# Performance work log

Measured on AMD Instinct MI355X. Metric: run time of the kernel, lower is better.

The kernel has to match this reference:

```python
import jax, jax.numpy as jnp
import numpy as np

D_MODEL = 1024
N_HEADS = 16
D_HEAD = D_MODEL // N_HEADS


def setup_inputs() -> dict:
    key = jax.random.key(0)
    k1, k2, k3 = jax.random.split(key, 3)
    B, T = 4, 2048
    x = jax.random.normal(k1, (B, T, D_MODEL), dtype=jnp.float32)
    # torch Linear(d, 3d, bias=False): y = x @ W.T ; we store W already transposed -> [d, 3d]
    w_qkv = jax.random.normal(k2, (D_MODEL, 3 * D_MODEL), dtype=jnp.float32) * (D_MODEL ** -0.5)
    w_proj = jax.random.normal(k3, (D_MODEL, D_MODEL), dtype=jnp.float32) * (D_MODEL ** -0.5)
    return {"x": x, "w_qkv": w_qkv, "w_proj": w_proj}


def reference(x, w_qkv, w_proj):
    B, T, C = x.shape
    H, Dh = N_HEADS, D_HEAD
    qkv = (x @ w_qkv).reshape(B, T, 3, H, Dh)
    q = jnp.transpose(qkv[:, :, 0], (0, 2, 1, 3))  # [B,H,T,Dh]
    k = jnp.transpose(qkv[:, :, 1], (0, 2, 1, 3))
    v = jnp.transpose(qkv[:, :, 2], (0, 2, 1, 3))
    scale = 1.0 / jnp.sqrt(jnp.asarray(Dh, dtype=x.dtype))
    att = jnp.einsum('bhqd,bhkd->bhqk', q, k) * scale  # [B,H,T,T]
    causal = jnp.tril(jnp.ones((T, T), dtype=bool))
    att = jnp.where(causal[None, None], att, jnp.asarray(-jnp.inf, dtype=att.dtype))
    att = jax.nn.softmax(att, axis=-1)
    y = jnp.einsum('bhqk,bhkd->bhqd', att, v)          # [B,H,T,Dh]
    y = jnp.transpose(y, (0, 2, 1, 3)).reshape(B, T, C)
    return y @ w_proj
```

## Files before the change

### kernel.cpp

```cpp
#include <hip/hip_runtime.h>
#include <hip/hip_bf16.h>
#include <cmath>

#define T_SEQ 2048
#define NHEADS 16
#define DHEAD 64
#define DMODEL 1024
#define CQKV 3072

typedef __attribute__((ext_vector_type(8))) short short8;
typedef __attribute__((ext_vector_type(8))) __bf16 bf16x8;
typedef __attribute__((ext_vector_type(4))) float floatx4;

#define LDS_CAST(p) ((__attribute__((address_space(3))) void*)(p))
#define GLB_CAST(p) ((const __attribute__((address_space(1))) void*)(p))

static __device__ __forceinline__ floatx4 mfma_bf16(short8 a, short8 b, floatx4 c) {
  return __builtin_amdgcn_mfma_f32_16x16x32_bf16(
      __builtin_bit_cast(bf16x8, a), __builtin_bit_cast(bf16x8, b), c, 0, 0, 0);
}

static __device__ __forceinline__ short f2bf(float f) {
  union { float f; unsigned u; } x; x.f = f;
  unsigned r = x.u + 0x7FFFu + ((x.u >> 16) & 1u);
  return (short)(r >> 16);
}

static __device__ __forceinline__ float bf2f(short s) {
  return __builtin_bit_cast(float, ((unsigned)(unsigned short)s) << 16);
}

static __device__ __forceinline__ float exp2_(float x) {
#if __has_builtin(__builtin_amdgcn_exp2f)
  return __builtin_amdgcn_exp2f(x);
#else
  return exp2f(x);
#endif
}

static __device__ __forceinline__ bool sniff_is_bf16(const unsigned* __restrict__ x) {
  int cnt = 0;
#pragma unroll
  for (int i = 0; i < 32; ++i) {
    unsigned e = (x[i] >> 7) & 0xFFu;
    cnt += (e >= 0x70u && e <= 0x8Fu) ? 1 : 0;
  }
  return cnt >= 16;
}

static __device__ __forceinline__ short8 load8f32(const char* p, size_t idx) {
  const float4* f = (const float4*)(p + idx * 4);
  float4 a = f[0], b = f[1];
  short8 r;
  r[0] = f2bf(a.x); r[1] = f2bf(a.y); r[2] = f2bf(a.z); r[3] = f2bf(a.w);
  r[4] = f2bf(b.x); r[5] = f2bf(b.y); r[6] = f2bf(b.z); r[7] = f2bf(b.w);
  return r;
}

__global__ __launch_bounds__(256) void conv_x(const char* __restrict__ x,
                                              short* __restrict__ o, int n,
                                              const unsigned* __restrict__ xs) {
  const bool isbf = sniff_is_bf16(xs);
  const int i = (blockIdx.x * 256 + threadIdx.x) * 8;
  if (i >= n) return;
  if (isbf) *(short8*)(o + i) = *(const short8*)((const short*)x + i);
  else      *(short8*)(o + i) = load8f32(x, (size_t)i);
}

__global__ __launch_bounds__(256) void tpose(const char* __restrict__ w,
                                             short* __restrict__ wt, int K, int N,
                                             const unsigned* __restrict__ xs) {
  const bool isbf = sniff_is_bf16(xs);
  __shared__ short tile[32][33];
  const int n0 = blockIdx.x * 32, k0 = blockIdx.y * 32;
  const int tx = threadIdx.x & 31, ty = threadIdx.x >> 5;
#pragma unroll
  for (int i = 0; i < 4; ++i) {
    const int r = ty * 4 + i;
    const size_t off = (size_t)(k0 + r) * N + n0 + tx;
    tile[r][tx] = isbf ? ((const short*)w)[off] : f2bf(((const float*)w)[off]);
  }
  __syncthreads();
#pragma unroll
  for (int i = 0; i < 4; ++i) {
    const int r = ty * 4 + i;
    wt[(size_t)(n0 + r) * K + k0 + tx] = tile[tx][r];
  }
}

__global__ __launch_bounds__(512) void gemm256(const short* __restrict__ A,
                                               const short* __restrict__ Bt,
                                               void* __restrict__ C,
                                               short* __restrict__ C2,
                                               int M, int N, int K, int mode,
                                               const unsigned* __restrict__ xs) {
  const bool out_f32 = (mode == 1) ? !sniff_is_bf16(xs) : false;

  __shared__ short as[2][256 * 64];
  __shared__ short bs[2][256 * 64];
  const int tid = threadIdx.x;
  const int wid = tid >> 6, lane = tid & 63;
  const int quad = lane >> 4, l16 = lane & 15;
  const int wm = wid >> 2, wn = wid & 3;

  const int gx = (int)gridDim.x;
  const int nwg = gx * (int)gridDim.y;
  int bid = (int)blockIdx.y * gx + (int)blockIdx.x;
  bid = (bid & 7) * (nwg >> 3) + (bid >> 3);
  const int m0 = (bid / gx) * 256;
  const int n0 = (bid % gx) * 256;

  const int srl = lane >> 3;
  const int sch = ((lane & 7) ^ srl) * 8;
  const int NT = K >> 6;

#define STAGE_A(t, h, b)                                                          \
  do {                                                                            \
    const int kt_ = (t) << 6;                                                     \
    _Pragma("unroll") for (int j_ = 0; j_ < 2; ++j_) {                            \
      const int row_ = (h) * 128 + j_ * 64 + wid * 8;                             \
      const short* g_ = A + (size_t)(m0 + row_ + srl) * K + kt_ + sch;            \
      __builtin_amdgcn_global_load_lds(GLB_CAST(g_), LDS_CAST(&as[(b)][row_ * 64]), 16, 0, 0); \
    }                                                                             \
  } while (0)

#define STAGE_B(t, h, b)                                                          \
  do {                                                                            \
    const int kt_ = (t) << 6;                                                     \
    _Pragma("unroll") for (int j_ = 0; j_ < 2; ++j_) {                            \
      const int row_ = (h) * 128 + j_ * 64 + wid * 8;                             \
      const short* g_ = Bt + (size_t)(n0 + row_ + srl) * K + kt_ + sch;           \
      __builtin_amdgcn_global_load_lds(GLB_CAST(g_), LDS_CAST(&bs[(b)][row_ * 64]), 16, 0, 0); \
    }                                                                             \
  } while (0)

#define SLOT_(kc) ((((kc) * 4 + quad) ^ (l16 & 7)) * 8)

#define LOAD_A(dst, mh, b)                                                        \
  do {                                                                            \
    _Pragma("unroll") for (int mf_ = 0; mf_ < 4; ++mf_)                           \
    _Pragma("unroll") for (int kc_ = 0; kc_ < 2; ++kc_)                           \
      dst[mf_][kc_] = *(const short8*)&as[(b)][(wm * 128 + (mh) * 64 + mf_ * 16 + l16) * 64 + SLOT_(kc_)]; \
  } while (0)

#define LOAD_B(dst, nh, b)                                                        \
  do {                                                                            \
    _Pragma("unroll") for (int nf_ = 0; nf_ < 2; ++nf_)                           \
    _Pragma("unroll") for (int kc_ = 0; kc_ < 2; ++kc_)                           \
      dst[nf_][kc_] = *(const short8*)&bs[(b)][(wn * 64 + (nh) * 32 + nf_ * 16 + l16) * 64 + SLOT_(kc_)]; \
  } while (0)

#define QMFMA(afrag, bfrag, mh, nh)                                               \
  do {                                                                            \
    __builtin_amdgcn_s_setprio(1);                                                \
    _Pragma("unroll") for (int mf_ = 0; mf_ < 4; ++mf_)                           \
    _Pragma("unroll") for (int nf_ = 0; nf_ < 2; ++nf_)                           \
    _Pragma("unroll") for (int kc_ = 0; kc_ < 2; ++kc_)                           \
      acc[(mh) * 4 + mf_][(nh) * 2 + nf_] =                                       \
          mfma_bf16(afrag[mf_][kc_], bfrag[nf_][kc_], acc[(mh) * 4 + mf_][(nh) * 2 + nf_]); \
    __builtin_amdgcn_s_setprio(0);                                                \
  } while (0)

#define BARW_()                                                                   \
  do {                                                                            \
    __builtin_amdgcn_s_barrier();                                                 \
    asm volatile("s_waitcnt lgkmcnt(0)" ::: "memory");                            \
  } while (0)

  const floatx4 zero4 = {0.f, 0.f, 0.f, 0.f};
  floatx4 acc[8][4];
#pragma unroll
  for (int i = 0; i < 8; ++i)
#pragma unroll
    for (int j = 0; j < 4; ++j) acc[i][j] = zero4;

  STAGE_B(0, 0, 0); STAGE_B(0, 1, 0);
  STAGE_A(0, 0, 0); STAGE_A(0, 1, 0);
  STAGE_B(1, 0, 1); STAGE_B(1, 1, 1);
  asm volatile("s_waitcnt vmcnt(4)" ::: "memory");
  __builtin_amdgcn_s_barrier();

  short8 afr[4][2], bf0[2][2], bf1[2][2];

  for (int t = 0; t < NT; ++t) {
    const int cb = t & 1, nb = cb ^ 1;
    const int tA = (t + 1 < NT) ? t + 1 : NT - 1;
    const int tB = (t + 2 < NT) ? t + 2 : NT - 1;

    LOAD_A(afr, 0, cb);
    LOAD_B(bf0, 0, cb);
    STAGE_A(tA, 0, nb);
    BARW_();
    QMFMA(afr, bf0, 0, 0);
    __builtin_amdgcn_s_barrier();

    LOAD_B(bf1, 1, cb);
    STAGE_A(tA, 1, nb);
    BARW_();
    QMFMA(afr, bf1, 0, 1);
    __builtin_amdgcn_s_barrier();

    LOAD_A(afr, 1, cb);
    STAGE_B(tB, 0, cb);
    BARW_();
    QMFMA(afr, bf1, 1, 1);
    __builtin_amdgcn_s_barrier();

    STAGE_B(tB, 1, cb);
    asm volatile("s_waitcnt vmcnt(4)" ::: "memory");
    BARW_();
    QMFMA(afr, bf0, 1, 0);
    __builtin_amdgcn_s_barrier();
  }
  asm volatile("s_waitcnt vmcnt(0)" ::: "memory");

  const int row0 = m0 + wm * 128 + quad * 4;
  const int col0 = n0 + wn * 64 + l16;
  if (mode == 2 && n0 >= 2048) {
#pragma unroll
    for (int mi = 0; mi < 8; ++mi)
#pragma unroll
      for (int ni = 0; ni < 4; ++ni)
#pragma unroll
        for (int r = 0; r < 4; ++r) {
          const int row = row0 + mi * 16 + r;
          const int col = col0 + ni * 16;
          const int d = col & 63, hh = (col >> 6) - 32;
          const int bb = row >> 11, tq = row & 2047;
          C2[((size_t)(bb * 16 + hh) * 64 + d) * T_SEQ + tq] = f2bf(acc[mi][ni][r]);
        }
  } else {
    const int outN = (mode == 2) ? 2048 : N;
#pragma unroll
    for (int mi = 0; mi < 8; ++mi)
#pragma unroll
      for (int ni = 0; ni < 4; ++ni)
#pragma unroll
        for (int r = 0; r < 4; ++r) {
          const size_t off = (size_t)(row0 + mi * 16 + r) * outN + col0 + ni * 16;
          if (out_f32) ((float*)C)[off] = acc[mi][ni][r];
          else         ((short*)C)[off] = f2bf(acc[mi][ni][r]);
        }
  }
#undef STAGE_A
#undef STAGE_B
#undef SLOT_
#undef LOAD_A
#undef LOAD_B
#undef QMFMA
#undef BARW_
}

__global__ __launch_bounds__(256) void attn(const short* __restrict__ qk,
                                            const short* __restrict__ vT,
                                            short* __restrict__ y) {
  __shared__ short ks[64 * 64];
  __shared__ short vs[64 * 64];
  __shared__ short ps[4][16][72];
  const int tid = threadIdx.x;
  const int wid = tid >> 6, lane = tid & 63;
  const int quad = lane >> 4, l16 = lane & 15;
  const int b = blockIdx.x >> 4, h = blockIdx.x & 15;
  const int q0 = ((int)gridDim.y - 1 - (int)blockIdx.y) * 64;
  const int qw0 = q0 + wid * 16;

  const short* qbase = qk + (size_t)b * T_SEQ * 2048 + h * DHEAD;
  const short* kbase = qbase + DMODEL;
  const short* vtb = vT + (size_t)(b * NHEADS + h) * DHEAD * T_SEQ;
  const float SC = 0.18033688011112042f;

  short8 aq[2];
#pragma unroll
  for (int kc = 0; kc < 2; ++kc) {
    short8 raw = *(const short8*)(qbase + (size_t)(qw0 + l16) * 2048 + kc * 32 + quad * 8);
#pragma unroll
    for (int j = 0; j < 8; ++j) aq[kc][j] = f2bf(bf2f(raw[j]) * SC);
  }

  const floatx4 zero4 = {0.f, 0.f, 0.f, 0.f};
  floatx4 o[4], lacc = zero4;
#pragma unroll
  for (int i = 0; i < 4; ++i) o[i] = zero4;
  const short8 ones8 = {0x3F80, 0x3F80, 0x3F80, 0x3F80, 0x3F80, 0x3F80, 0x3F80, 0x3F80};

  const int srl = lane >> 3;
  const int sch = ((lane & 7) ^ srl) * 8;

  const int kend = q0 + 64;
  for (int kt = 0; kt < kend; kt += 64) {
    __syncthreads();
#pragma unroll
    for (int i = 0; i < 2; ++i) {
      const int row = i * 32 + wid * 8 + srl;
      const short* gk = kbase + (size_t)(kt + row) * 2048 + sch;
      const short* gv = vtb + (size_t)row * T_SEQ + kt + sch;
      __builtin_amdgcn_global_load_lds(GLB_CAST(gk), LDS_CAST(ks + (i * 32 + wid * 8) * 64), 16, 0, 0);
      __builtin_amdgcn_global_load_lds(GLB_CAST(gv), LDS_CAST(vs + (i * 32 + wid * 8) * 64), 16, 0, 0);
    }
    __syncthreads();

    floatx4 s[4];
#pragma unroll
    for (int nt = 0; nt < 4; ++nt) {
      s[nt] = zero4;
#pragma unroll
      for (int kc = 0; kc < 2; ++kc) {
        const int slot = ((kc * 4 + quad) ^ (l16 & 7)) * 8;
        const short8 bk = *(const short8*)&ks[(nt * 16 + l16) * 64 + slot];
        s[nt] = mfma_bf16(aq[kc], bk, s[nt]);
      }
    }

    const bool full = (kt + 63 <= qw0);
#pragma unroll
    for (int nt = 0; nt < 4; ++nt)
#pragma unroll
      for (int r = 0; r < 4; ++r) {
        float p = exp2_(s[nt][r]);
        if (!full) {
          const int key = kt + nt * 16 + l16;
          const int q = qw0 + quad * 4 + r;
          p = (key <= q) ? p : 0.f;
        }
        s[nt][r] = p;
      }

#pragma unroll
    for (int nt = 0; nt < 4; ++nt)
#pragma unroll
      for (int r = 0; r < 4; ++r)
        ps[wid][quad * 4 + r][nt * 16 + l16] = f2bf(s[nt][r]);

#pragma unroll
    for (int kc = 0; kc < 2; ++kc) {
      const short8 ap = *(const short8*)&ps[wid][l16][kc * 32 + quad * 8];
      lacc = mfma_bf16(ap, ones8, lacc);
#pragma unroll
      for (int d4 = 0; d4 < 4; ++d4) {
        const int slot = ((kc * 4 + quad) ^ (l16 & 7)) * 8;
        const short8 bv = *(const short8*)&vs[(d4 * 16 + l16) * 64 + slot];
        o[d4] = mfma_bf16(ap, bv, o[d4]);
      }
    }
  }

  floatx4 inv;
#pragma unroll
  for (int r = 0; r < 4; ++r) inv[r] = 1.0f / lacc[r];
#pragma unroll
  for (int d4 = 0; d4 < 4; ++d4)
#pragma unroll
    for (int r = 0; r < 4; ++r) {
      const int q = qw0 + quad * 4 + r;
      y[(size_t)(b * T_SEQ + q) * DMODEL + h * DHEAD + d4 * 16 + l16] =
          f2bf(o[d4][r] * inv[r]);
    }
}

extern "C" void kernel_launch(void* const* d_in, const int* in_sizes, int n_in,
                              void* d_out, int out_size, void* d_ws, size_t ws_size,
                              hipStream_t stream) {
  const char* x = (const char*)d_in[0];
  const char* w_qkv = (const char*)d_in[1];
  const char* w_proj = (const char*)d_in[2];
  const unsigned* xs = (const unsigned*)d_in[0];

  short* qk = (short*)d_ws;
  short* vTb = qk + (size_t)8192 * 2048;
  short* wqkvT = vTb + (size_t)64 * 64 * 2048;
  short* wprojT = wqkvT + (size_t)3072 * 1024;
  short* xbf = wprojT + (size_t)1024 * 1024;
  short* ybuf = xbf;

  conv_x<<<8192 * 1024 / (256 * 8), 256, 0, stream>>>(x, xbf, 8192 * 1024, xs);
  {
    dim3 g1(3072 / 32, 1024 / 32);
    tpose<<<g1, 256, 0, stream>>>(w_qkv, wqkvT, 1024, 3072, xs);
    dim3 g2(1024 / 32, 1024 / 32);
    tpose<<<g2, 256, 0, stream>>>(w_proj, wprojT, 1024, 1024, xs);
  }
  {
    dim3 grid(3072 / 256, 8192 / 256);
    gemm256<<<grid, 512, 0, stream>>>(xbf, wqkvT, qk, vTb, 8192, 3072, 1024, 2, xs);
  }
  {
    dim3 grid(4 * NHEADS, T_SEQ / 64);
    attn<<<grid, 256, 0, stream>>>(qk, vTb, ybuf);
  }
  {
    dim3 grid(1024 / 256, 8192 / 256);
    gemm256<<<grid, 512, 0, stream>>>(ybuf, wprojT, d_out, nullptr, 8192, 1024, 1024, 1, xs);
  }
}
```

Baseline: 282.9 us.

## Double-buffer K/V tiles in attention and use a 128-tile projection GEMM

```diff
diff --git a/kernel.cpp b/kernel.cpp
--- a/kernel.cpp
+++ b/kernel.cpp
@@ -251,11 +251,97 @@
 #undef BARW_
 }
 
+__global__ __launch_bounds__(256) void gemm128(const short* __restrict__ A,
+                                               const short* __restrict__ Bt,
+                                               void* __restrict__ C,
+                                               short* __restrict__ C2,
+                                               int M, int N, int K, int mode,
+                                               const unsigned* __restrict__ xs) {
+  const bool out_f32 = (mode == 1) ? !sniff_is_bf16(xs) : false;
+
+  __shared__ short as[128 * 64];
+  __shared__ short bs[128 * 64];
+  const int tid = threadIdx.x;
+  const int wid = tid >> 6, lane = tid & 63;
+  const int quad = lane >> 4, l16 = lane & 15;
+  const int wm = wid >> 1, wn = wid & 1;
+  const int m0 = blockIdx.y * 128, n0 = blockIdx.x * 128;
+
+  const int srl = lane >> 3;
+  const int sch = ((lane & 7) ^ srl) * 8;
+
+  const floatx4 zero4 = {0.f, 0.f, 0.f, 0.f};
+  floatx4 acc[4][4];
+#pragma unroll
+  for (int i = 0; i < 4; ++i)
+#pragma unroll
+    for (int j = 0; j < 4; ++j) acc[i][j] = zero4;
+
+  for (int kt = 0; kt < K; kt += 64) {
+    __syncthreads();
+#pragma unroll
+    for (int i = 0; i < 4; ++i) {
+      const int row = wid * 32 + i * 8;
+      const short* ga = A + (size_t)(m0 + row + srl) * K + kt + sch;
+      const short* gb = Bt + (size_t)(n0 + row + srl) * K + kt + sch;
+      __builtin_amdgcn_global_load_lds(GLB_CAST(ga), LDS_CAST(as + row * 64), 16, 0, 0);
+      __builtin_amdgcn_global_load_lds(GLB_CAST(gb), LDS_CAST(bs + row * 64), 16, 0, 0);
+    }
+    __syncthreads();
+
+#pragma unroll
+    for (int kc = 0; kc < 2; ++kc) {
+      const int slot = ((kc * 4 + quad) ^ (l16 & 7)) * 8;
+      short8 afr[4], bfr[4];
+#pragma unroll
+      for (int mt = 0; mt < 4; ++mt)
+        afr[mt] = *(const short8*)&as[(wm * 64 + mt * 16 + l16) * 64 + slot];
+#pragma unroll
+      for (int nt = 0; nt < 4; ++nt)
+        bfr[nt] = *(const short8*)&bs[(wn * 64 + nt * 16 + l16) * 64 + slot];
+#pragma unroll
+      for (int mt = 0; mt < 4; ++mt)
+#pragma unroll
+        for (int nt = 0; nt < 4; ++nt)
+          acc[mt][nt] = mfma_bf16(afr[mt], bfr[nt], acc[mt][nt]);
+    }
+  }
+
+  const int row0 = m0 + wm * 64 + quad * 4;
+  const int col0 = n0 + wn * 64 + l16;
+  if (mode == 2 && n0 >= 2048) {
+#pragma unroll
+    for (int mt = 0; mt < 4; ++mt)
+#pragma unroll
+      for (int nt = 0; nt < 4; ++nt)
+#pragma unroll
+        for (int r = 0; r < 4; ++r) {
+          const int row = row0 + mt * 16 + r;
+          const int col = col0 + nt * 16;
+          const int d = col & 63, hh = (col >> 6) - 32;
+          const int bb = row >> 11, t = row & 2047;
+          C2[((size_t)(bb * 16 + hh) * 64 + d) * T_SEQ + t] = f2bf(acc[mt][nt][r]);
+        }
+  } else {
+    const int outN = (mode == 2) ? 2048 : N;
+#pragma unroll
+    for (int mt = 0; mt < 4; ++mt)
+#pragma unroll
+      for (int nt = 0; nt < 4; ++nt)
+#pragma unroll
+        for (int r = 0; r < 4; ++r) {
+          const size_t off = (size_t)(row0 + mt * 16 + r) * outN + col0 + nt * 16;
+          if (out_f32) ((float*)C)[off] = acc[mt][nt][r];
+          else         ((short*)C)[off] = f2bf(acc[mt][nt][r]);
+        }
+  }
+}
+
 __global__ __launch_bounds__(256) void attn(const short* __restrict__ qk,
                                             const short* __restrict__ vT,
                                             short* __restrict__ y) {
-  __shared__ short ks[64 * 64];
-  __shared__ short vs[64 * 64];
+  __shared__ short ks[2][64 * 64];
+  __shared__ short vs[2][64 * 64];
   __shared__ short ps[4][16][72];
   const int tid = threadIdx.x;
   const int wid = tid >> 6, lane = tid & 63;
@@ -269,6 +355,9 @@
   const short* vtb = vT + (size_t)(b * NHEADS + h) * DHEAD * T_SEQ;
   const float SC = 0.18033688011112042f;
 
+  const int srl = lane >> 3;
+  const int sch = ((lane & 7) ^ srl) * 8;
+
   short8 aq[2];
 #pragma unroll
   for (int kc = 0; kc < 2; ++kc) {
@@ -283,21 +372,35 @@
   for (int i = 0; i < 4; ++i) o[i] = zero4;
   const short8 ones8 = {0x3F80, 0x3F80, 0x3F80, 0x3F80, 0x3F80, 0x3F80, 0x3F80, 0x3F80};
 
-  const int srl = lane >> 3;
-  const int sch = ((lane & 7) ^ srl) * 8;
-
   const int kend = q0 + 64;
-  for (int kt = 0; kt < kend; kt += 64) {
+
+#pragma unroll
+  for (int i = 0; i < 2; ++i) {
+    const int row = i * 32 + wid * 8 + srl;
+    const short* gk = kbase + (size_t)row * 2048 + sch;
+    const short* gv = vtb + (size_t)row * T_SEQ + sch;
+    __builtin_amdgcn_global_load_lds(GLB_CAST(gk), LDS_CAST(&ks[0][(i * 32 + wid * 8) * 64]), 16, 0, 0);
+    __builtin_amdgcn_global_load_lds(GLB_CAST(gv), LDS_CAST(&vs[0][(i * 32 + wid * 8) * 64]), 16, 0, 0);
+  }
+
+  int cur = 0;
+  for (int kt = 0; kt < kend; kt += 64, cur ^= 1) {
     __syncthreads();
-#pragma unroll
-    for (int i = 0; i < 2; ++i) {
-      const int row = i * 32 + wid * 8 + srl;
-      const short* gk = kbase + (size_t)(kt + row) * 2048 + sch;
-      const short* gv = vtb + (size_t)row * T_SEQ + kt + sch;
-      __builtin_amdgcn_global_load_lds(GLB_CAST(gk), LDS_CAST(ks + (i * 32 + wid * 8) * 64), 16, 0, 0);
-      __builtin_amdgcn_global_load_lds(GLB_CAST(gv), LDS_CAST(vs + (i * 32 + wid * 8) * 64), 16, 0, 0);
-    }
-    __syncthreads();
+
+    if (kt + 64 < kend) {
+      const int nxt = cur ^ 1;
+#pragma unroll
+      for (int i = 0; i < 2; ++i) {
+        const int row = i * 32 + wid * 8 + srl;
+        const short* gk = kbase + (size_t)(kt + 64 + row) * 2048 + sch;
+        const short* gv = vtb + (size_t)row * T_SEQ + kt + 64 + sch;
+        __builtin_amdgcn_global_load_lds(GLB_CAST(gk), LDS_CAST(&ks[nxt][(i * 32 + wid * 8) * 64]), 16, 0, 0);
+        __builtin_amdgcn_global_load_lds(GLB_CAST(gv), LDS_CAST(&vs[nxt][(i * 32 + wid * 8) * 64]), 16, 0, 0);
+      }
+    }
+
+    const short* ksc = &ks[cur][0];
+    const short* vsc = &vs[cur][0];
 
     floatx4 s[4];
 #pragma unroll
@@ -306,7 +409,7 @@
 #pragma unroll
       for (int kc = 0; kc < 2; ++kc) {
         const int slot = ((kc * 4 + quad) ^ (l16 & 7)) * 8;
-        const short8 bk = *(const short8*)&ks[(nt * 16 + l16) * 64 + slot];
+        const short8 bk = *(const short8*)&ksc[(nt * 16 + l16) * 64 + slot];
         s[nt] = mfma_bf16(aq[kc], bk, s[nt]);
       }
     }
@@ -338,7 +441,7 @@
 #pragma unroll
       for (int d4 = 0; d4 < 4; ++d4) {
         const int slot = ((kc * 4 + quad) ^ (l16 & 7)) * 8;
-        const short8 bv = *(const short8*)&vs[(d4 * 16 + l16) * 64 + slot];
+        const short8 bv = *(const short8*)&vsc[(d4 * 16 + l16) * 64 + slot];
         o[d4] = mfma_bf16(ap, bv, o[d4]);
       }
     }
@@ -388,7 +491,7 @@
     attn<<<grid, 256, 0, stream>>>(qk, vTb, ybuf);
   }
   {
-    dim3 grid(1024 / 256, 8192 / 256);
-    gemm256<<<grid, 512, 0, stream>>>(ybuf, wprojT, d_out, nullptr, 8192, 1024, 1024, 1, xs);
-  }
-}
+    dim3 grid(1024 / 128, 8192 / 128);
+    gemm128<<<grid, 256, 0, stream>>>(ybuf, wprojT, d_out, nullptr, 8192, 1024, 1024, 1, xs);
+  }
+}
```

Result: faster. 273.4 us (-3.3%).
